# Kernel optimization log

Hardware: AMD Instinct MI355X
Metric: run time of the kernel (lower is better)

The kernel has to match this reference:

```python
import jax, jax.numpy as jnp
import numpy as np

D_MODEL = 1024
NUM_HEADS = 16
D_STATE = D_MODEL // NUM_HEADS
BS, SEQ = 8, 1024
NEG_BIG = 1e10


def setup_inputs() -> dict:
    key = jax.random.key(0)
    ks = jax.random.split(key, 3)
    std = 0.02
    x = jax.random.normal(ks[0], (BS, SEQ, D_MODEL), dtype=jnp.float32)
    qkv_w = jax.random.normal(ks[1], (D_MODEL, 3 * D_MODEL), dtype=jnp.float32) * std
    qkv_b = jnp.zeros((3 * D_MODEL,), dtype=jnp.float32)
    out_w = jax.random.normal(ks[2], (D_MODEL, D_MODEL), dtype=jnp.float32) * std
    out_b = jnp.zeros((D_MODEL,), dtype=jnp.float32)
    return {"x": x, "qkv_w": qkv_w, "qkv_b": qkv_b, "out_w": out_w, "out_b": out_b}


def reference(x, qkv_w, qkv_b, out_w, out_b):
    bs, n, d = x.shape
    qkv = jnp.matmul(x, qkv_w) + qkv_b  # [bs, n, 3*d_model]
    q, k, v = jnp.split(qkv, 3, axis=-1)

    def split_heads(t):  # [bs, n, d] -> [bs, h, n, d_state]
        return t.reshape(bs, n, NUM_HEADS, D_STATE).transpose(0, 2, 1, 3)

    q, k, v = split_heads(q), split_heads(k), split_heads(v)
    scale = 1.0 / np.sqrt(D_STATE).astype(np.float32)
    scores = jnp.einsum('bhqd,bhkd->bhqk', q, k) * scale  # [bs,h,n,n]
    # causal mask: i >= j (mask(n) with ns==nd)
    m = (jnp.arange(n)[:, None] >= jnp.arange(n)[None, :]).astype(scores.dtype)
    scores = scores * m - (1.0 - m) * NEG_BIG
    attn = jax.nn.softmax(scores, axis=-1)
    out = jnp.einsum('bhqk,bhkd->bhqd', attn, v)  # [bs,h,n,d_state]
    out = out.transpose(0, 2, 1, 3).reshape(bs, n, d)
    return jnp.matmul(out, out_w) + out_b
```

## Files before the change

### kernel.cpp

```cpp
#include <hip/hip_runtime.h>
#include <hip/hip_bf16.h>
#include <stdint.h>

typedef __attribute__((ext_vector_type(8))) __bf16 bf16x8;
typedef __attribute__((ext_vector_type(4))) float f32x4;
typedef __attribute__((ext_vector_type(4))) unsigned int u32x4;
typedef __attribute__((ext_vector_type(4))) unsigned short u16x4;

#define SEQ 1024
#define DM 1024

#if __has_builtin(__builtin_amdgcn_exp2f)
#define EXP2(x) __builtin_amdgcn_exp2f(x)
#else
#define EXP2(x) exp2f(x)
#endif

typedef __attribute__((address_space(3))) void lds_t;
typedef __attribute__((address_space(1))) void glb_t;

__device__ __forceinline__ unsigned short f2bf(float f){
  __hip_bfloat16 h = __float2bfloat16(f);
  return __builtin_bit_cast(unsigned short, h);
}
__device__ __forceinline__ bf16x8 ld16(const unsigned short* p){
  u32x4 v = *(const u32x4*)p;
  return __builtin_bit_cast(bf16x8, v);
}
__device__ __forceinline__ void gload_lds16(const unsigned short* g, unsigned short* l){
  __builtin_amdgcn_global_load_lds((const glb_t*)g, (lds_t*)l, 16, 0, 0);
}

__global__ void cvt_f32_bf16(const float* __restrict__ in,
                             unsigned short* __restrict__ out, int n)
{
  int i = (blockIdx.x * blockDim.x + threadIdx.x) * 8;
  if (i >= n) return;
  float4 a = *(const float4*)(in + i);
  float4 b = *(const float4*)(in + i + 4);
  unsigned short v[8] = { f2bf(a.x), f2bf(a.y), f2bf(a.z), f2bf(a.w),
                          f2bf(b.x), f2bf(b.y), f2bf(b.z), f2bf(b.w) };
  *(u32x4*)(out + i) = *(u32x4*)v;
}

__global__ void transpose_cvt(const float* __restrict__ in,
                              unsigned short* __restrict__ out, int R, int C)
{
  __shared__ unsigned short t[32][33];
  int x  = blockIdx.x * 32 + threadIdx.x;
  int y0 = blockIdx.y * 32 + threadIdx.y;
#pragma unroll
  for (int i = 0; i < 32; i += 8)
    t[threadIdx.y + i][threadIdx.x] = f2bf(in[(size_t)(y0 + i) * C + x]);
  __syncthreads();
  int ox  = blockIdx.y * 32 + threadIdx.x;
  int oy0 = blockIdx.x * 32 + threadIdx.y;
#pragma unroll
  for (int i = 0; i < 32; i += 8)
    out[(size_t)(oy0 + i) * R + ox] = t[threadIdx.x][threadIdx.y + i];
}

__global__ __launch_bounds__(256, 2)
void gemm_qkv(const unsigned short* __restrict__ A,
              const unsigned short* __restrict__ Bt,
              const float* __restrict__ bias,
              unsigned short* __restrict__ qko, unsigned short* __restrict__ vT,
              int M, int N, int K)
{
  __shared__ unsigned short As[3][128 * 32];
  __shared__ unsigned short Bs[3][192 * 32];
  const int tid = threadIdx.x;
  const int l = tid & 63;
  const int w = tid >> 6;

  const int nbn = N / 192;
  const int nwg = gridDim.x;
  const int bid = blockIdx.x;
  const int qq  = nwg >> 3;
  const int sb  = (bid & 7) * qq + (bid >> 3);
  const int bm = sb / nbn, bn = sb % nbn;
  const int row0 = bm << 7, col0 = bn * 192;

  const int rs = tid >> 2;
  const int cS = ((tid & 3) ^ ((tid >> 3) & 3)) * 8;
  const unsigned short* ag = A  + (size_t)(row0 + rs) * K + cS;
  const unsigned short* bg = Bt + (size_t)(col0 + rs) * K + cS;

  auto STAGE = [&](int kt, int bi) {
    const unsigned short* a = ag + kt * 32;
    const unsigned short* b = bg + kt * 32;
    gload_lds16(a,                   &As[bi][w * 512]);
    gload_lds16(a + (size_t)64 * K,  &As[bi][2048 + w * 512]);
    gload_lds16(b,                   &Bs[bi][w * 512]);
    gload_lds16(b + (size_t)64 * K,  &Bs[bi][2048 + w * 512]);
    gload_lds16(b + (size_t)128 * K, &Bs[bi][4096 + w * 512]);
  };

  const int wr = (w >> 1) * 64;
  const int wc = (w & 1) * 96;
  const f32x4 zz = {0.f, 0.f, 0.f, 0.f};
  f32x4 acc[4][6];
#pragma unroll
  for (int m = 0; m < 4; m++)
#pragma unroll
    for (int n = 0; n < 6; n++) acc[m][n] = zz;

  const int c16 = l & 15;
  const int csw = ((l >> 4) * 8) ^ (((l >> 1) & 3) << 3);

  const int NT = K >> 5;
  STAGE(0, 0);
  STAGE(1, 1);
  asm volatile("s_waitcnt vmcnt(5)" ::: "memory");
  __builtin_amdgcn_s_barrier();

  int cur = 0, stg = 2;
  for (int kt = 0; kt < NT; kt++) {
    if (kt + 2 < NT) STAGE(kt + 2, stg);

    bf16x8 af[4], bfr[6];
#pragma unroll
    for (int m = 0; m < 4; m++)
      af[m] = ld16(&As[cur][(wr + m * 16 + c16) * 32 + csw]);
#pragma unroll
    for (int n = 0; n < 6; n++)
      bfr[n] = ld16(&Bs[cur][(wc + n * 16 + c16) * 32 + csw]);
#pragma unroll
    for (int m = 0; m < 4; m++)
#pragma unroll
      for (int n = 0; n < 6; n++)
        acc[m][n] = __builtin_amdgcn_mfma_f32_16x16x32_bf16(af[m], bfr[n], acc[m][n], 0, 0, 0);

    if (kt + 1 < NT) {
      if (kt + 2 < NT) asm volatile("s_waitcnt vmcnt(5)" ::: "memory");
      else             asm volatile("s_waitcnt vmcnt(0)" ::: "memory");
      __builtin_amdgcn_s_barrier();
    }
    cur = (cur == 2) ? 0 : cur + 1;
    stg = (stg == 2) ? 0 : stg + 1;
  }

#pragma unroll
  for (int n = 0; n < 6; n++) {
    int col = col0 + wc + n * 16 + c16;
    float bv = bias[col];
#pragma unroll
    for (int m = 0; m < 4; m++) {
      int rbase = row0 + wr + m * 16 + (l >> 4) * 4;
      if (col < 2048) {
        float sc = (col < 1024) ? 0.18033688f : 1.0f;
#pragma unroll
        for (int r = 0; r < 4; r++)
          qko[(size_t)(rbase + r) * 2048 + col] = f2bf((acc[m][n][r] + bv) * sc);
      } else {
        int bb = rbase >> 10, s0v = rbase & 1023;
        int hh = (col - 2048) >> 6, dd = (col - 2048) & 63;
        u16x4 pk;
#pragma unroll
        for (int r = 0; r < 4; r++) pk[r] = f2bf(acc[m][n][r] + bv);
        *(u16x4*)(vT + ((size_t)((bb * 16 + hh) * 64 + dd)) * 1024 + s0v) = pk;
      }
    }
  }
}

__global__ __launch_bounds__(256, 3)
void gemm_out(const unsigned short* __restrict__ A,
              const unsigned short* __restrict__ Bt,
              const float* __restrict__ bias,
              float* __restrict__ C, int M, int N, int K)
{
  __shared__ unsigned short Ls[3][2][128 * 32];
  const int tid = threadIdx.x;
  const int l = tid & 63;
  const int w = tid >> 6;

  const int nbn = N >> 7;
  const int nwg = gridDim.x;
  const int bid = blockIdx.x;
  const int qq  = nwg >> 3;
  const int sb  = (bid & 7) * qq + (bid >> 3);
  const int bm = sb / nbn, bn = sb % nbn;
  const int row0 = bm << 7, col0 = bn << 7;

  const int rA = w * 16 + (l >> 2);
  const int cS = ((l & 3) ^ ((l >> 3) & 3)) * 8;
  const unsigned short* ag = A  + (size_t)(row0 + rA) * K + cS;
  const unsigned short* bg = Bt + (size_t)(col0 + rA) * K + cS;

  auto STAGE = [&](int kt, int bi) {
    const unsigned short* a = ag + kt * 32;
    const unsigned short* b = bg + kt * 32;
    gload_lds16(a,                  &Ls[bi][0][w * 512]);
    gload_lds16(a + (size_t)64 * K, &Ls[bi][0][2048 + w * 512]);
    gload_lds16(b,                  &Ls[bi][1][w * 512]);
    gload_lds16(b + (size_t)64 * K, &Ls[bi][1][2048 + w * 512]);
  };

  const int wr = (w >> 1) * 64, wc = (w & 1) * 64;
  const f32x4 zz = {0.f, 0.f, 0.f, 0.f};
  f32x4 acc[4][4];
#pragma unroll
  for (int m = 0; m < 4; m++)
#pragma unroll
    for (int n = 0; n < 4; n++) acc[m][n] = zz;

  const int c16 = l & 15;
  const int csw = ((l >> 4) * 8) ^ (((l >> 1) & 3) << 3);

  const int NT = K >> 5;
  STAGE(0, 0);
  STAGE(1, 1);
  asm volatile("s_waitcnt vmcnt(4)" ::: "memory");
  __builtin_amdgcn_s_barrier();

  int cur = 0, stg = 2;
  for (int kt = 0; kt < NT; kt++) {
    if (kt + 2 < NT) STAGE(kt + 2, stg);

    const unsigned short* La = &Ls[cur][0][0];
    const unsigned short* Lb = &Ls[cur][1][0];
    bf16x8 af[4], bfr[4];
#pragma unroll
    for (int m = 0; m < 4; m++)
      af[m] = ld16(La + (wr + m * 16 + c16) * 32 + csw);
#pragma unroll
    for (int n = 0; n < 4; n++)
      bfr[n] = ld16(Lb + (wc + n * 16 + c16) * 32 + csw);
#pragma unroll
    for (int m = 0; m < 4; m++)
#pragma unroll
      for (int n = 0; n < 4; n++)
        acc[m][n] = __builtin_amdgcn_mfma_f32_16x16x32_bf16(af[m], bfr[n], acc[m][n], 0, 0, 0);

    if (kt + 1 < NT) {
      if (kt + 2 < NT) asm volatile("s_waitcnt vmcnt(4)" ::: "memory");
      else             asm volatile("s_waitcnt vmcnt(0)" ::: "memory");
      __builtin_amdgcn_s_barrier();
    }
    cur = (cur == 2) ? 0 : cur + 1;
    stg = (stg == 2) ? 0 : stg + 1;
  }

#pragma unroll
  for (int n = 0; n < 4; n++) {
    int col = col0 + wc + n * 16 + c16;
    float bv = bias[col];
#pragma unroll
    for (int m = 0; m < 4; m++) {
      int rbase = row0 + wr + m * 16 + (l >> 4) * 4;
#pragma unroll
      for (int r = 0; r < 4; r++)
        C[(size_t)(rbase + r) * N + col] = acc[m][n][r] + bv;
    }
  }
}

__global__ __launch_bounds__(256, 2)
void attn(const unsigned short* __restrict__ qk,
          const unsigned short* __restrict__ vT,
          unsigned short* __restrict__ ctx)
{
  __shared__ unsigned short Ksh[3][64 * 64];
  __shared__ unsigned short Ps[4][32 * 64];
  const int tid = threadIdx.x;
  const int l = tid & 63, w = tid >> 6;

  const int lin = blockIdx.x + (blockIdx.y << 2);
  const int xcd = lin & 7;
  const int j   = lin >> 3;
  const int bh  = xcd * 16 + (j & 15);
  const int bx  = j >> 4;
  const int b = bh >> 4, h = bh & 15;

  const unsigned short* qbase = qk + (size_t)b * SEQ * 2048;
  const unsigned short* kbase = qbase + 1024 + h * 64;
  const unsigned short* vbase = vT + (size_t)bh * 64 * 1024;
  unsigned short* Psw = Ps[w];
  const int d8 = (l >> 4) * 8;
  const int c16 = l & 15;
  const int r4 = (l >> 4) * 4;
  const int kvr = w * 8 + (l >> 3);
  const int cb  = (l & 7) * 16;

  const int qbA = 7 - bx, qbB = bx;
  const int q0A = qbA * 128 + w * 32, q0B = qbB * 128 + w * 32;
  const int ntA = (qbA + 1) * 2;
  const int kmaxA = (q0A + 31) >> 6, kmaxB = (q0B + 31) >> 6;

  bf16x8 qaA[2][2], qaB[2][2];
#pragma unroll
  for (int qc = 0; qc < 2; qc++)
#pragma unroll
    for (int kg = 0; kg < 2; kg++) {
      qaA[qc][kg] = ld16(qbase + (size_t)(q0A + qc * 16 + c16) * 2048
                               + h * 64 + kg * 32 + d8);
      qaB[qc][kg] = ld16(qbase + (size_t)(q0B + qc * 16 + c16) * 2048
                               + h * 64 + kg * 32 + d8);
    }

  const f32x4 zz = {0.f, 0.f, 0.f, 0.f};
  f32x4 oA[2][4], oB[2][4];
#pragma unroll
  for (int m = 0; m < 2; m++)
#pragma unroll
    for (int n = 0; n < 4; n++) { oA[m][n] = zz; oB[m][n] = zz; }
  float mA[2] = {-1e30f, -1e30f}, lA[2] = {0.f, 0.f};
  float mB[2] = {-1e30f, -1e30f}, lB[2] = {0.f, 0.f};

  auto STAGEK = [&](int t, int bufi) {
#pragma unroll
    for (int i = 0; i < 2; i++) {
      int row = i * 32 + kvr;
      int srcb = cb ^ ((row & 7) << 4);
      gload_lds16(kbase + (size_t)(t * 64 + row) * 2048 + (srcb >> 1),
                  &Ksh[bufi][i * 2048 + w * 512]);
    }
  };

  auto QK = [&](const unsigned short* Kc, bf16x8 (&qa)[2][2], f32x4 (&st)[4][2]) {
    bf16x8 kb[4];
    int bo0 = ((d8) * 2) ^ ((c16 & 7) << 4);
    int bo1 = (((32 + d8)) * 2) ^ ((c16 & 7) << 4);
#pragma unroll
    for (int mt = 0; mt < 4; mt++)
      kb[mt] = ld16(Kc + (mt * 16 + c16) * 64 + (bo0 >> 1));
#pragma unroll
    for (int mt = 0; mt < 4; mt++)
#pragma unroll
      for (int qc = 0; qc < 2; qc++)
        st[mt][qc] = __builtin_amdgcn_mfma_f32_16x16x32_bf16(kb[mt], qa[qc][0], zz, 0, 0, 0);
#pragma unroll
    for (int mt = 0; mt < 4; mt++)
      kb[mt] = ld16(Kc + (mt * 16 + c16) * 64 + (bo1 >> 1));
#pragma unroll
    for (int mt = 0; mt < 4; mt++)
#pragma unroll
      for (int qc = 0; qc < 2; qc++)
        st[mt][qc] = __builtin_amdgcn_mfma_f32_16x16x32_bf16(kb[mt], qa[qc][1], st[mt][qc], 0, 0, 0);
  };

  auto SMPV = [&](f32x4 (&st)[4][2], f32x4 (&o)[2][4], float (&mrun)[2],
                  float (&lrun)[2], int q0, int kvt,
                  bf16x8 (&vb0)[4], bf16x8 (&vb1)[4]) {
    if (kvt * 64 + 63 > q0) {
#pragma unroll
      for (int mt = 0; mt < 4; mt++)
#pragma unroll
        for (int qc = 0; qc < 2; qc++) {
          int qg = q0 + qc * 16 + c16;
#pragma unroll
          for (int r = 0; r < 4; r++) {
            int kvg = kvt * 64 + mt * 16 + r4 + r;
            if (kvg > qg) st[mt][qc][r] = -1e30f;
          }
        }
    }
    float plane[2];
#pragma unroll
    for (int qc = 0; qc < 2; qc++) {
      float mx = -1e30f;
#pragma unroll
      for (int mt = 0; mt < 4; mt++)
#pragma unroll
        for (int r = 0; r < 4; r++) mx = fmaxf(mx, st[mt][qc][r]);
      plane[qc] = mx;
    }
    int defer0 = __all(plane[0] - mrun[0] <= 11.5f);
    int defer1 = __all(plane[1] - mrun[1] <= 11.5f);
    float scq[2] = {1.f, 1.f};
#pragma unroll
    for (int qc = 0; qc < 2; qc++) {
      int defer = qc ? defer1 : defer0;
      if (!defer) {
        float mx = plane[qc];
        mx = fmaxf(mx, __shfl_xor(mx, 16));
        mx = fmaxf(mx, __shfl_xor(mx, 32));
        float mn = fmaxf(mrun[qc], mx);
        scq[qc] = EXP2(mrun[qc] - mn);
        mrun[qc] = mn;
      }
      float mn = mrun[qc];
      float rs = 0.f;
#pragma unroll
      for (int mt = 0; mt < 4; mt++)
#pragma unroll
        for (int r = 0; r < 4; r++) {
          float p = EXP2(st[mt][qc][r] - mn);
          st[mt][qc][r] = p;
          rs += p;
        }
      rs += __shfl_xor(rs, 16);
      rs += __shfl_xor(rs, 32);
      lrun[qc] = lrun[qc] * scq[qc] + rs;
    }
    if (!(defer0 && defer1)) {
#pragma unroll
      for (int m = 0; m < 2; m++)
#pragma unroll
        for (int r = 0; r < 4; r++) {
          float sc = __shfl(scq[m], (l & 48) | (r4 + r));
#pragma unroll
          for (int n = 0; n < 4; n++) o[m][n][r] *= sc;
        }
    }
#pragma unroll
    for (int qc = 0; qc < 2; qc++) {
      int rowl = qc * 16 + c16;
#pragma unroll
      for (int mt = 0; mt < 4; mt++) {
        int byteoff = ((mt * 16 + r4) * 2) ^ ((c16 & 7) << 4);
        u16x4 pk;
#pragma unroll
        for (int r = 0; r < 4; r++) pk[r] = f2bf(st[mt][qc][r]);
        *(u16x4*)(Psw + rowl * 64 + (byteoff >> 1)) = pk;
      }
    }
    bf16x8 pa[2];
    int bo0 = (d8 * 2) ^ ((c16 & 7) << 4);
    int bo1 = ((32 + d8) * 2) ^ ((c16 & 7) << 4);
#pragma unroll
    for (int m = 0; m < 2; m++)
      pa[m] = ld16(Psw + (m * 16 + c16) * 64 + (bo0 >> 1));
#pragma unroll
    for (int m = 0; m < 2; m++)
#pragma unroll
      for (int n = 0; n < 4; n++)
        o[m][n] = __builtin_amdgcn_mfma_f32_16x16x32_bf16(pa[m], vb0[n], o[m][n], 0, 0, 0);
#pragma unroll
    for (int m = 0; m < 2; m++)
      pa[m] = ld16(Psw + (m * 16 + c16) * 64 + (bo1 >> 1));
#pragma unroll
    for (int m = 0; m < 2; m++)
#pragma unroll
      for (int n = 0; n < 4; n++)
        o[m][n] = __builtin_amdgcn_mfma_f32_16x16x32_bf16(pa[m], vb1[n], o[m][n], 0, 0, 0);
  };

  STAGEK(0, 0);
  STAGEK(1, 1);
  asm volatile("s_waitcnt vmcnt(2)" ::: "memory");
  __builtin_amdgcn_s_barrier();

  int bufc = 0;
  for (int kvt = 0; kvt < ntA; kvt++) {
    const int bufn = bufc ? bufc - 1 : 2;
    const bool more = (kvt + 2 < ntA);
    if (more) STAGEK(kvt + 2, bufn);
    const unsigned short* Kc = Ksh[bufc];

    if (kvt <= kmaxA) {
      f32x4 st[4][2];
      QK(Kc, qaA, st);
      bf16x8 vb0[4], vb1[4];
#pragma unroll
      for (int n = 0; n < 4; n++) {
        vb0[n] = ld16(vbase + (size_t)(n * 16 + c16) * 1024 + kvt * 64 + d8);
        vb1[n] = ld16(vbase + (size_t)(n * 16 + c16) * 1024 + kvt * 64 + 32 + d8);
      }
      SMPV(st, oA, mA, lA, q0A, kvt, vb0, vb1);
      if (kvt <= kmaxB) {
        QK(Kc, qaB, st);
        SMPV(st, oB, mB, lB, q0B, kvt, vb0, vb1);
      }
    }

    if (more) asm volatile("s_waitcnt vmcnt(2)" ::: "memory");
    else      asm volatile("s_waitcnt vmcnt(0)" ::: "memory");
    __builtin_amdgcn_s_barrier();
    bufc = (bufc == 2) ? 0 : bufc + 1;
  }

  auto WRITE = [&](f32x4 (&o)[2][4], float (&lrun)[2], int q0) {
    float invq[2];
#pragma unroll
    for (int qc = 0; qc < 2; qc++) invq[qc] = 1.f / lrun[qc];
#pragma unroll
    for (int m = 0; m < 2; m++)
#pragma unroll
      for (int r = 0; r < 4; r++) {
        float inv = __shfl(invq[m], (l & 48) | (r4 + r));
        int qg = q0 + m * 16 + r4 + r;
#pragma unroll
        for (int n = 0; n < 4; n++) {
          int d = n * 16 + c16;
          ctx[(size_t)(b * SEQ + qg) * DM + h * 64 + d] = f2bf(o[m][n][r] * inv);
        }
      }
  };
  WRITE(oA, lA, q0A);
  WRITE(oB, lB, q0B);
}

extern "C" void kernel_launch(void* const* d_in, const int* in_sizes, int n_in,
                              void* d_out, int out_size, void* d_ws, size_t ws_size,
                              hipStream_t stream)
{
  const float* x     = (const float*)d_in[0];
  const float* qkv_w = (const float*)d_in[1];
  const float* qkv_b = (const float*)d_in[2];
  const float* out_w = (const float*)d_in[3];
  const float* out_b = (const float*)d_in[4];

  unsigned short* ws   = (unsigned short*)d_ws;
  unsigned short* xb   = ws;
  unsigned short* wqT  = xb  + (size_t)8192 * 1024;
  unsigned short* woT  = wqT + 3072 * 1024;
  unsigned short* qkb  = woT + 1024 * 1024;
  unsigned short* vTb  = qkb + (size_t)8192 * 2048;
  unsigned short* ctxb = vTb + (size_t)128 * 64 * 1024;

  hipLaunchKernelGGL(cvt_f32_bf16, dim3(8192 * 1024 / 8 / 256), dim3(256), 0, stream,
                     x, xb, 8192 * 1024);
  hipLaunchKernelGGL(transpose_cvt, dim3(3072 / 32, 1024 / 32), dim3(32, 8), 0, stream,
                     qkv_w, wqT, 1024, 3072);
  hipLaunchKernelGGL(transpose_cvt, dim3(1024 / 32, 1024 / 32), dim3(32, 8), 0, stream,
                     out_w, woT, 1024, 1024);
  hipLaunchKernelGGL(gemm_qkv, dim3(64 * 16), dim3(256), 0, stream,
                     xb, wqT, qkv_b, qkb, vTb, 8192, 3072, 1024);
  hipLaunchKernelGGL(attn, dim3(4, 128), dim3(256), 0, stream,
                     qkb, vTb, ctxb);
  hipLaunchKernelGGL(gemm_out, dim3(64 * 8), dim3(256), 0, stream,
                     ctxb, woT, out_b, (float*)d_out, 8192, 1024, 1024);
}
```

Measured before the change: 151.4 us.

## Load QKV GEMM B fragments directly from global into registers, shrink tile to 128x128

The QKV projection GEMM no longer stages the weight tile in LDS. Each wave loads its B fragments straight from global memory into registers and prefetches the next k-step. The tile drops from 128x192 to 128x128, giving more workgroups, and occupancy is raised to 3 blocks per SIMD. This cuts LDS traffic and footprint, at the cost of uncoalesced per-lane B loads, less reuse of B across waves, and trickier vmcnt accounting.

Result: slower. 194.1 us (+28.3%).

```diff
diff --git a/kernel.cpp b/kernel.cpp
--- a/kernel.cpp
+++ b/kernel.cpp
@@ -60,7 +60,7 @@
     out[(size_t)(oy0 + i) * R + ox] = t[threadIdx.x][threadIdx.y + i];
 }
 
-__global__ __launch_bounds__(256, 2)
+__global__ __launch_bounds__(256, 3)
 void gemm_qkv(const unsigned short* __restrict__ A,
               const unsigned short* __restrict__ Bt,
               const float* __restrict__ bias,
@@ -68,80 +68,85 @@
               int M, int N, int K)
 {
   __shared__ unsigned short As[3][128 * 32];
-  __shared__ unsigned short Bs[3][192 * 32];
   const int tid = threadIdx.x;
   const int l = tid & 63;
   const int w = tid >> 6;
 
-  const int nbn = N / 192;
+  const int nbn = N >> 7;
   const int nwg = gridDim.x;
   const int bid = blockIdx.x;
   const int qq  = nwg >> 3;
   const int sb  = (bid & 7) * qq + (bid >> 3);
   const int bm = sb / nbn, bn = sb % nbn;
-  const int row0 = bm << 7, col0 = bn * 192;
-
-  const int rs = tid >> 2;
-  const int cS = ((tid & 3) ^ ((tid >> 3) & 3)) * 8;
-  const unsigned short* ag = A  + (size_t)(row0 + rs) * K + cS;
-  const unsigned short* bg = Bt + (size_t)(col0 + rs) * K + cS;
+  const int row0 = bm << 7, col0 = bn << 7;
+
+  const int rA = w * 16 + (l >> 2);
+  const int cS = ((l & 3) ^ ((l >> 3) & 3)) * 8;
+  const unsigned short* ag = A + (size_t)(row0 + rA) * K + cS;
 
   auto STAGE = [&](int kt, int bi) {
     const unsigned short* a = ag + kt * 32;
-    const unsigned short* b = bg + kt * 32;
-    gload_lds16(a,                   &As[bi][w * 512]);
-    gload_lds16(a + (size_t)64 * K,  &As[bi][2048 + w * 512]);
-    gload_lds16(b,                   &Bs[bi][w * 512]);
-    gload_lds16(b + (size_t)64 * K,  &Bs[bi][2048 + w * 512]);
-    gload_lds16(b + (size_t)128 * K, &Bs[bi][4096 + w * 512]);
+    gload_lds16(a,                  &As[bi][w * 512]);
+    gload_lds16(a + (size_t)64 * K, &As[bi][2048 + w * 512]);
   };
 
-  const int wr = (w >> 1) * 64;
-  const int wc = (w & 1) * 96;
+  const int wr = (w >> 1) * 64, wc = (w & 1) * 64;
+  const int c16 = l & 15;
+  const int d8 = (l >> 4) * 8;
+  const int csw = d8 ^ (((l >> 1) & 3) << 3);
+
+  const unsigned short* bfb = Bt + (size_t)(col0 + wc + c16) * K + d8;
+
   const f32x4 zz = {0.f, 0.f, 0.f, 0.f};
-  f32x4 acc[4][6];
+  f32x4 acc[4][4];
 #pragma unroll
   for (int m = 0; m < 4; m++)
 #pragma unroll
-    for (int n = 0; n < 6; n++) acc[m][n] = zz;
-
-  const int c16 = l & 15;
-  const int csw = ((l >> 4) * 8) ^ (((l >> 1) & 3) << 3);
+    for (int n = 0; n < 4; n++) acc[m][n] = zz;
 
   const int NT = K >> 5;
+
+  bf16x8 bcur[4], bnext[4];
+#pragma unroll
+  for (int n = 0; n < 4; n++)
+    bcur[n] = ld16(bfb + (size_t)(n * 16) * K);
   STAGE(0, 0);
   STAGE(1, 1);
-  asm volatile("s_waitcnt vmcnt(5)" ::: "memory");
+  asm volatile("s_waitcnt vmcnt(2)" ::: "memory");
   __builtin_amdgcn_s_barrier();
 
   int cur = 0, stg = 2;
   for (int kt = 0; kt < NT; kt++) {
+    if (kt + 1 < NT) {
+#pragma unroll
+      for (int n = 0; n < 4; n++)
+        bnext[n] = ld16(bfb + (size_t)(n * 16) * K + (kt + 1) * 32);
+    }
     if (kt + 2 < NT) STAGE(kt + 2, stg);
 
-    bf16x8 af[4], bfr[6];
+    bf16x8 af[4];
 #pragma unroll
     for (int m = 0; m < 4; m++)
       af[m] = ld16(&As[cur][(wr + m * 16 + c16) * 32 + csw]);
 #pragma unroll
-    for (int n = 0; n < 6; n++)
-      bfr[n] = ld16(&Bs[cur][(wc + n * 16 + c16) * 32 + csw]);
-#pragma unroll
     for (int m = 0; m < 4; m++)
 #pragma unroll
-      for (int n = 0; n < 6; n++)
-        acc[m][n] = __builtin_amdgcn_mfma_f32_16x16x32_bf16(af[m], bfr[n], acc[m][n], 0, 0, 0);
+      for (int n = 0; n < 4; n++)
+        acc[m][n] = __builtin_amdgcn_mfma_f32_16x16x32_bf16(af[m], bcur[n], acc[m][n], 0, 0, 0);
 
     if (kt + 1 < NT) {
-      if (kt + 2 < NT) asm volatile("s_waitcnt vmcnt(5)" ::: "memory");
-      else             asm volatile("s_waitcnt vmcnt(0)" ::: "memory");
+      if (kt + 2 < NT) asm volatile("s_waitcnt vmcnt(6)" ::: "memory");
+      else             asm volatile("s_waitcnt vmcnt(4)" ::: "memory");
       __builtin_amdgcn_s_barrier();
+#pragma unroll
+      for (int n = 0; n < 4; n++) bcur[n] = bnext[n];
     }
     cur = (cur == 2) ? 0 : cur + 1;
     stg = (stg == 2) ? 0 : stg + 1;
   }
 
 #pragma unroll
-  for (int n = 0; n < 6; n++) {
+  for (int n = 0; n < 4; n++) {
     int col = col0 + wc + n * 16 + c16;
     float bv = bias[col];
 #pragma unroll
@@ -516,7 +521,7 @@
                      qkv_w, wqT, 1024, 3072);
   hipLaunchKernelGGL(transpose_cvt, dim3(1024 / 32, 1024 / 32), dim3(32, 8), 0, stream,
                      out_w, woT, 1024, 1024);
-  hipLaunchKernelGGL(gemm_qkv, dim3(64 * 16), dim3(256), 0, stream,
+  hipLaunchKernelGGL(gemm_qkv, dim3(64 * 24), dim3(256), 0, stream,
                      xb, wqT, qkv_b, qkb, vTb, 8192, 3072, 1024);
   hipLaunchKernelGGL(attn, dim3(4, 128), dim3(256), 0, stream,
                      qkb, vTb, ctxb);
```
